# Kernel optimization log

Measured on AMD Instinct MI355X. Metric: run time of the kernel, lower is better.

The kernel has to match this reference:

```python
import jax, jax.numpy as jnp
import numpy as np


def setup_inputs() -> dict:
    key = jax.random.key(0)
    k1, k2, k3, k4 = jax.random.split(key, 4)
    B, T, C, H = 4, 4096, 1024, 64
    x = jax.random.normal(k1, (B, T, C), dtype=jnp.float32)
    Wq = jax.random.normal(k2, (C, H), dtype=jnp.float32) * (C ** -0.5)
    Wk = jax.random.normal(k3, (C, H), dtype=jnp.float32) * (C ** -0.5)
    Wv = jax.random.normal(k4, (C, H), dtype=jnp.float32) * (C ** -0.5)
    return {"x": x, "Wq": Wq, "Wk": Wk, "Wv": Wv}


def reference(x, Wq, Wk, Wv):
    B, T, C = x.shape
    q = jnp.einsum('btc,ch->bth', x, Wq)  # [B,T,H]
    k = jnp.einsum('btc,ch->bth', x, Wk)
    v = jnp.einsum('btc,ch->bth', x, Wv)
    # NOTE: original scales by C**0.5 (embed_dim), not head_size**0.5
    scale = jnp.asarray(C, x.dtype) ** 0.5
    wei = jnp.einsum('bth,bsh->bts', q, k) / scale  # [B,T,T]
    causal = jnp.tril(jnp.ones((T, T), dtype=bool))
    wei = jnp.where(causal, wei, -jnp.inf)
    wei = jax.nn.softmax(wei, axis=-1)  # dropout p=0.0 -> identity
    return jnp.einsum('bts,bsh->bth', wei, v)  # [B,T,H]
```

## Files before the change

kernel.cpp:

```cpp
#include <hip/hip_runtime.h>
#include <hip/hip_bf16.h>

typedef __bf16 bf16;
typedef __bf16 bf16x8 __attribute__((ext_vector_type(8)));
typedef __bf16 bf16x4 __attribute__((ext_vector_type(4)));
typedef float  f32x4  __attribute__((ext_vector_type(4)));

#define MFMA16(A, B, C) __builtin_amdgcn_mfma_f32_16x16x32_bf16((A), (B), (C), 0, 0, 0)

static constexpr int Bn = 4;
static constexpr int T  = 4096;
static constexpr int Cd = 1024;
static constexpr int H  = 64;
static constexpr int NG = 192;
static constexpr int CH = 8;
static constexpr int SLOTS_PER_B = 288;
static constexpr float QSCALE = 0.03125f;

__device__ inline void dma16(const void* g, void* l) {
    __builtin_amdgcn_global_load_lds(
        (const __attribute__((address_space(1))) unsigned int*)g,
        (__attribute__((address_space(3))) unsigned int*)l, 16, 0, 0);
}

__device__ inline bf16x8 cvt_bf16x8(float4 a, float4 b) {
    bf16x8 r;
    r[0] = (bf16)a.x; r[1] = (bf16)a.y; r[2] = (bf16)a.z; r[3] = (bf16)a.w;
    r[4] = (bf16)b.x; r[5] = (bf16)b.y; r[6] = (bf16)b.z; r[7] = (bf16)b.w;
    return r;
}

__global__ __launch_bounds__(256) void wt_kernel(const float* __restrict__ Wq,
                                                 const float* __restrict__ Wk,
                                                 const float* __restrict__ Wv,
                                                 bf16* __restrict__ Wt) {
    __shared__ float s[64][65];
    const int cb = blockIdx.x;
    const int m  = blockIdx.y;
    const float* W = (m == 0) ? Wq : (m == 1) ? Wk : Wv;
    for (int i = threadIdx.x; i < 64 * 64; i += 256) {
        const int c = i >> 6, h = i & 63;
        s[c][h] = W[(cb * 64 + c) * H + h];
    }
    __syncthreads();
    for (int i = threadIdx.x; i < 64 * 64; i += 256) {
        const int n = i >> 6, c = i & 63;
        Wt[(m * 64 + n) * Cd + cb * 64 + c] = (bf16)s[c][n];
    }
}

__global__ __launch_bounds__(512, 4) void proj_kernel(const float* __restrict__ x,
                                                      const bf16* __restrict__ Wt,
                                                      bf16* __restrict__ qw,
                                                      bf16* __restrict__ kw,
                                                      bf16* __restrict__ vtw) {
    const int tid  = threadIdx.x;
    const int lane = tid & 63;
    const int w    = tid >> 6;
    const int wr   = w >> 2;
    const int wc   = w & 3;
    const int ml   = lane & 15;
    const int quad = lane >> 4;

    const long r0 = (long)blockIdx.x * 32;

    __shared__ float sX[2][32][64];
    __shared__ bf16  sW[2][192][64];

    const int xrow = w * 4 + (lane >> 4);
    const float* gx = x + (r0 + xrow) * Cd + (((lane & 15) ^ (xrow & 15)) << 2);
    const int wchunk = ((lane & 7) ^ (lane >> 3)) << 3;
    const bf16* gw0 = Wt + (long)(w * 24 + 0 + (lane >> 3)) * Cd + wchunk;
    const bf16* gw1 = Wt + (long)(w * 24 + 8 + (lane >> 3)) * Cd + wchunk;
    const bf16* gw2 = Wt + (long)(w * 24 + 16 + (lane >> 3)) * Cd + wchunk;

    f32x4 acc[3];
    #pragma unroll
    for (int j = 0; j < 3; ++j) acc[j] = f32x4{0.f, 0.f, 0.f, 0.f};

    dma16(gx, &sX[0][w * 4][0]);
    dma16(gw0, &sW[0][w * 24 + 0][0]);
    dma16(gw1, &sW[0][w * 24 + 8][0]);
    dma16(gw2, &sW[0][w * 24 + 16][0]);
    __syncthreads();

    const int arow = wr * 16 + ml;
    const int brow0 = wc * 48 + ml;
    const int bsw = ml & 7;

    int buf = 0;
    for (int kb = 0; kb < Cd; kb += 64) {
        if (kb + 64 < Cd) {
            dma16(gx + kb + 64, &sX[buf ^ 1][w * 4][0]);
            dma16(gw0 + kb + 64, &sW[buf ^ 1][w * 24 + 0][0]);
            dma16(gw1 + kb + 64, &sW[buf ^ 1][w * 24 + 8][0]);
            dma16(gw2 + kb + 64, &sW[buf ^ 1][w * 24 + 16][0]);
        }

        #pragma unroll
        for (int ks = 0; ks < 2; ++ks) {
            const int ca = (ks * 8 + quad * 2) ^ ml;
            const float4 lo = *(const float4*)&sX[buf][arow][ca << 2];
            const float4 hi = *(const float4*)&sX[buf][arow][(ca ^ 1) << 2];
            const bf16x8 af = cvt_bf16x8(lo, hi);
            const int cb0 = (ks * 4 + quad) ^ bsw;
            acc[0] = MFMA16(af, *(const bf16x8*)&sW[buf][brow0 + 0][cb0 << 3], acc[0]);
            acc[1] = MFMA16(af, *(const bf16x8*)&sW[buf][brow0 + 16][cb0 << 3], acc[1]);
            acc[2] = MFMA16(af, *(const bf16x8*)&sW[buf][brow0 + 32][cb0 << 3], acc[2]);
        }

        __syncthreads();
        buf ^= 1;
    }

    const int b = (int)(r0 >> 12);
    const long rowb = r0 + wr * 16 + quad * 4;
    const int  tloc = (int)(rowb & 4095);

    #pragma unroll
    for (int f = 0; f < 3; ++f) {
        const int base = wc * 48 + f * 16;
        const int sel  = base >> 6;
        const int h    = (base & 63) + ml;
        if (sel == 0) {
            #pragma unroll
            for (int rr = 0; rr < 4; ++rr)
                qw[(rowb + rr) * H + h] = (bf16)(acc[f][rr] * QSCALE);
        } else if (sel == 1) {
            #pragma unroll
            for (int rr = 0; rr < 4; ++rr)
                kw[(rowb + rr) * H + h] = (bf16)acc[f][rr];
        } else {
            bf16x4 pv;
            #pragma unroll
            for (int rr = 0; rr < 4; ++rr) pv[rr] = (bf16)acc[f][rr];
            *(bf16x4*)(vtw + ((long)(b * H + h)) * T + tloc) = pv;
        }
    }
}

__global__ __launch_bounds__(256, 3) void attn_kernel(const bf16* __restrict__ qw,
                                                      const bf16* __restrict__ kw,
                                                      const bf16* __restrict__ vtw,
                                                      float* __restrict__ pO,
                                                      float* __restrict__ pL) {
    const int qt = blockIdx.x;
    const int c  = blockIdx.y;
    const int b  = blockIdx.z;
    const int g  = qt >> 3, r = qt & 7;
    if (c > g) return;

    const int tid  = threadIdx.x;
    const int lane = tid & 63;
    const int w    = tid >> 6;
    const int ml   = lane & 15;
    const int quad = lane >> 4;
    const int mx   = ml & 7;

    __shared__ bf16 sK[2][64][64];
    __shared__ bf16 sVt[2][64][64];
    __shared__ bf16 sP[4][16][72];

    const int t0 = qt * 64;

    const bf16* q0 = qw + ((long)b * T + t0 + w * 16 + ml) * H;
    const bf16x8 aq0 = *(const bf16x8*)(q0 + quad * 8);
    const bf16x8 aq1 = *(const bf16x8*)(q0 + 32 + quad * 8);

    f32x4 O[4];
    #pragma unroll
    for (int ht = 0; ht < 4; ++ht) O[ht] = f32x4{0.f, 0.f, 0.f, 0.f};
    float lrow[4] = {0.f, 0.f, 0.f, 0.f};

    const int trow = t0 + w * 16 + quad * 4;
    const int jt0 = c * CH;
    const int jt1 = (c == g) ? qt + 1 : (c + 1) * CH;

    const int drow = w * 8 + (lane >> 3);
    const int dsw  = ((lane & 7) ^ (drow & 7)) << 3;
    const bf16* kbase = kw + (long)b * T * H;
    const bf16* vbase = vtw + (long)b * H * T;
    const long koffA = (long)drow * H + dsw;
    const long koffB = koffA + 32 * H;
    const long voffA = (long)drow * T + dsw;
    const long voffB = voffA + (long)32 * T;

    {
        const long ks0 = (long)jt0 * 64;
        dma16(kbase + ks0 * H + koffA, &sK[0][w * 8][0]);
        dma16(kbase + ks0 * H + koffB, &sK[0][32 + w * 8][0]);
        dma16(vbase + ks0 + voffA, &sVt[0][w * 8][0]);
        dma16(vbase + ks0 + voffB, &sVt[0][32 + w * 8][0]);
    }
    __syncthreads();

    int buf = 0;
    for (int jt = jt0; jt < jt1; ++jt) {
        if (jt + 1 < jt1) {
            const long ksn = (long)(jt + 1) * 64;
            dma16(kbase + ksn * H + koffA, &sK[buf ^ 1][w * 8][0]);
            dma16(kbase + ksn * H + koffB, &sK[buf ^ 1][32 + w * 8][0]);
            dma16(vbase + ksn + voffA, &sVt[buf ^ 1][w * 8][0]);
            dma16(vbase + ksn + voffB, &sVt[buf ^ 1][32 + w * 8][0]);
        }

        const int s0 = jt * 64;
        const bool diag = (jt == qt);
        #pragma unroll
        for (int nt = 0; nt < 4; ++nt) {
            f32x4 sacc = f32x4{0.f, 0.f, 0.f, 0.f};
            sacc = MFMA16(aq0, *(const bf16x8*)&sK[buf][nt * 16 + ml][(quad ^ mx) << 3], sacc);
            sacc = MFMA16(aq1, *(const bf16x8*)&sK[buf][nt * 16 + ml][((4 + quad) ^ mx) << 3], sacc);
            const int col = s0 + nt * 16 + ml;
            #pragma unroll
            for (int rr = 0; rr < 4; ++rr) {
                const float p = (diag && col > trow + rr) ? 0.f : __expf(sacc[rr]);
                lrow[rr] += p;
                sP[w][quad * 4 + rr][nt * 16 + ml] = (bf16)p;
            }
        }
        asm volatile("s_waitcnt lgkmcnt(0)" ::: "memory");

        #pragma unroll
        for (int ks = 0; ks < 2; ++ks) {
            const bf16x8 ap = *(const bf16x8*)&sP[w][ml][ks * 32 + quad * 8];
            #pragma unroll
            for (int ht = 0; ht < 4; ++ht)
                O[ht] = MFMA16(ap,
                    *(const bf16x8*)&sVt[buf][ht * 16 + ml][(((ks << 2) + quad) ^ mx) << 3],
                    O[ht]);
        }

        __syncthreads();
        buf ^= 1;
    }

    #pragma unroll
    for (int d = 1; d < 16; d <<= 1)
        #pragma unroll
        for (int rr = 0; rr < 4; ++rr)
            lrow[rr] += __shfl_xor(lrow[rr], d, 64);

    const long slot = (long)b * SLOTS_PER_B + (long)(g + 1) * (4 * g + r) + c;
    float* po = pO + slot * 4096 + (w * 16) * 64;
    #pragma unroll
    for (int ht = 0; ht < 4; ++ht)
        #pragma unroll
        for (int rr = 0; rr < 4; ++rr)
            po[(quad * 4 + rr) * 64 + ht * 16 + ml] = O[ht][rr];
    if (ml == 0) {
        #pragma unroll
        for (int rr = 0; rr < 4; ++rr)
            pL[slot * 64 + w * 16 + quad * 4 + rr] = lrow[rr];
    }
}

__global__ __launch_bounds__(256) void combine_kernel(const float* __restrict__ pO,
                                                      const float* __restrict__ pL,
                                                      float* __restrict__ out) {
    const int qt = blockIdx.x;
    const int b  = blockIdx.y;
    const int g  = qt >> 3, r = qt & 7;
    const int nch = g + 1;
    const long slot0 = (long)b * SLOTS_PER_B + (long)(g + 1) * (4 * g + r);

    const int tid = threadIdx.x;
    const int row = tid >> 2;
    const int q4  = tid & 3;

    f32x4 o[4];
    #pragma unroll
    for (int j = 0; j < 4; ++j) o[j] = f32x4{0.f, 0.f, 0.f, 0.f};
    float l = 0.f;

    for (int cc = 0; cc < nch; ++cc) {
        const float* po = pO + (slot0 + cc) * 4096 + row * 64 + q4 * 16;
        #pragma unroll
        for (int j = 0; j < 4; ++j) o[j] += *(const f32x4*)(po + j * 4);
        l += pL[(slot0 + cc) * 64 + row];
    }
    const float inv = 1.f / l;
    float* op = out + ((long)b * T + qt * 64 + row) * H + q4 * 16;
    #pragma unroll
    for (int j = 0; j < 4; ++j) {
        f32x4 v = o[j];
        v[0] *= inv; v[1] *= inv; v[2] *= inv; v[3] *= inv;
        *(f32x4*)(op + j * 4) = v;
    }
}

extern "C" void kernel_launch(void* const* d_in, const int* in_sizes, int n_in,
                              void* d_out, int out_size, void* d_ws, size_t ws_size,
                              hipStream_t stream) {
    const float* x  = (const float*)d_in[0];
    const float* Wq = (const float*)d_in[1];
    const float* Wk = (const float*)d_in[2];
    const float* Wv = (const float*)d_in[3];
    float* out = (float*)d_out;

    char* ws = (char*)d_ws;
    const size_t WT_BYTES = (size_t)NG * Cd * sizeof(bf16);
    const size_t QK_BYTES = (size_t)Bn * T * H * sizeof(bf16);
    const size_t PO_OFF   = WT_BYTES + 3 * QK_BYTES;
    const size_t PO_BYTES = (size_t)Bn * SLOTS_PER_B * 4096 * sizeof(float);
    bf16*  Wt  = (bf16*)ws;
    bf16*  qw  = (bf16*)(ws + WT_BYTES);
    bf16*  kw  = (bf16*)(ws + WT_BYTES + QK_BYTES);
    bf16*  vtw = (bf16*)(ws + WT_BYTES + 2 * QK_BYTES);
    float* pO  = (float*)(ws + PO_OFF);
    float* pL  = (float*)(ws + PO_OFF + PO_BYTES);

    wt_kernel<<<dim3(16, 3), dim3(256), 0, stream>>>(Wq, Wk, Wv, Wt);
    proj_kernel<<<dim3((Bn * T) / 32), dim3(512), 0, stream>>>(x, Wt, qw, kw, vtw);
    attn_kernel<<<dim3(T / 64, CH, Bn), dim3(256), 0, stream>>>(qw, kw, vtw, pO, pL);
    combine_kernel<<<dim3(T / 64, Bn), dim3(256), 0, stream>>>(pO, pL, out);
}
```

Measured before the change: 153.4 us.

## Triple-buffer DMA pipelines in projection and attention, enlarge proj tile, split combine

```diff
diff --git a/kernel.cpp b/kernel.cpp
--- a/kernel.cpp
+++ b/kernel.cpp
@@ -7,6 +7,8 @@
 typedef float  f32x4  __attribute__((ext_vector_type(4)));
 
 #define MFMA16(A, B, C) __builtin_amdgcn_mfma_f32_16x16x32_bf16((A), (B), (C), 0, 0, 0)
+#define WAITV(N) asm volatile("s_waitcnt vmcnt(" #N ")" ::: "memory")
+#define BARRIER() asm volatile("s_barrier" ::: "memory")
 
 static constexpr int Bn = 4;
 static constexpr int T  = 4096;
@@ -49,7 +51,7 @@
     }
 }
 
-__global__ __launch_bounds__(512, 4) void proj_kernel(const float* __restrict__ x,
+__global__ __launch_bounds__(512, 2) void proj_kernel(const float* __restrict__ x,
                                                       const bf16* __restrict__ Wt,
                                                       bf16* __restrict__ qw,
                                                       bf16* __restrict__ kw,
@@ -62,84 +64,105 @@
     const int ml   = lane & 15;
     const int quad = lane >> 4;
 
-    const long r0 = (long)blockIdx.x * 32;
-
-    __shared__ float sX[2][32][64];
-    __shared__ bf16  sW[2][192][64];
-
-    const int xrow = w * 4 + (lane >> 4);
-    const float* gx = x + (r0 + xrow) * Cd + (((lane & 15) ^ (xrow & 15)) << 2);
-    const int wchunk = ((lane & 7) ^ (lane >> 3)) << 3;
-    const bf16* gw0 = Wt + (long)(w * 24 + 0 + (lane >> 3)) * Cd + wchunk;
-    const bf16* gw1 = Wt + (long)(w * 24 + 8 + (lane >> 3)) * Cd + wchunk;
-    const bf16* gw2 = Wt + (long)(w * 24 + 16 + (lane >> 3)) * Cd + wchunk;
-
-    f32x4 acc[3];
-    #pragma unroll
-    for (int j = 0; j < 3; ++j) acc[j] = f32x4{0.f, 0.f, 0.f, 0.f};
-
-    dma16(gx, &sX[0][w * 4][0]);
-    dma16(gw0, &sW[0][w * 24 + 0][0]);
+    const long r0 = (long)blockIdx.x * 64;
+
+    __shared__ float sX[3][64][64];
+    __shared__ bf16  sW[3][192][64];
+
+    const int xr0 = w * 8 + (lane >> 4);
+    const int xch = lane & 15;
+    const float* gx0 = x + (r0 + xr0) * Cd + ((xch ^ (xr0 & 15)) << 2);
+    const float* gx1 = x + (r0 + xr0 + 4) * Cd + ((xch ^ ((xr0 + 4) & 15)) << 2);
+    const int wr8 = lane >> 3;
+    const int wsw = ((lane & 7) ^ wr8) << 3;
+    const bf16* gw0 = Wt + (long)(w * 24 + 0  + wr8) * Cd + wsw;
+    const bf16* gw1 = Wt + (long)(w * 24 + 8  + wr8) * Cd + wsw;
+    const bf16* gw2 = Wt + (long)(w * 24 + 16 + wr8) * Cd + wsw;
+
+    f32x4 acc[2][3];
+    #pragma unroll
+    for (int g = 0; g < 2; ++g)
+        #pragma unroll
+        for (int f = 0; f < 3; ++f) acc[g][f] = f32x4{0.f, 0.f, 0.f, 0.f};
+
+    dma16(gx0, &sX[0][w * 8][0]);
+    dma16(gx1, &sX[0][w * 8 + 4][0]);
+    dma16(gw0, &sW[0][w * 24][0]);
     dma16(gw1, &sW[0][w * 24 + 8][0]);
     dma16(gw2, &sW[0][w * 24 + 16][0]);
-    __syncthreads();
-
-    const int arow = wr * 16 + ml;
-    const int brow0 = wc * 48 + ml;
-    const int bsw = ml & 7;
-
-    int buf = 0;
+    dma16(gx0 + 64, &sX[1][w * 8][0]);
+    dma16(gx1 + 64, &sX[1][w * 8 + 4][0]);
+    dma16(gw0 + 64, &sW[1][w * 24][0]);
+    dma16(gw1 + 64, &sW[1][w * 24 + 8][0]);
+    dma16(gw2 + 64, &sW[1][w * 24 + 16][0]);
+
+    int bi = 0;
     for (int kb = 0; kb < Cd; kb += 64) {
-        if (kb + 64 < Cd) {
-            dma16(gx + kb + 64, &sX[buf ^ 1][w * 4][0]);
-            dma16(gw0 + kb + 64, &sW[buf ^ 1][w * 24 + 0][0]);
-            dma16(gw1 + kb + 64, &sW[buf ^ 1][w * 24 + 8][0]);
-            dma16(gw2 + kb + 64, &sW[buf ^ 1][w * 24 + 16][0]);
+        if (kb != Cd - 64) WAITV(5);
+        else               WAITV(0);
+        BARRIER();
+        if (kb + 128 < Cd) {
+            const int bn = (bi >= 1) ? bi - 1 : 2;
+            const int kn = kb + 128;
+            dma16(gx0 + kn, &sX[bn][w * 8][0]);
+            dma16(gx1 + kn, &sX[bn][w * 8 + 4][0]);
+            dma16(gw0 + kn, &sW[bn][w * 24][0]);
+            dma16(gw1 + kn, &sW[bn][w * 24 + 8][0]);
+            dma16(gw2 + kn, &sW[bn][w * 24 + 16][0]);
         }
 
         #pragma unroll
         for (int ks = 0; ks < 2; ++ks) {
             const int ca = (ks * 8 + quad * 2) ^ ml;
-            const float4 lo = *(const float4*)&sX[buf][arow][ca << 2];
-            const float4 hi = *(const float4*)&sX[buf][arow][(ca ^ 1) << 2];
-            const bf16x8 af = cvt_bf16x8(lo, hi);
-            const int cb0 = (ks * 4 + quad) ^ bsw;
-            acc[0] = MFMA16(af, *(const bf16x8*)&sW[buf][brow0 + 0][cb0 << 3], acc[0]);
-            acc[1] = MFMA16(af, *(const bf16x8*)&sW[buf][brow0 + 16][cb0 << 3], acc[1]);
-            acc[2] = MFMA16(af, *(const bf16x8*)&sW[buf][brow0 + 32][cb0 << 3], acc[2]);
-        }
-
-        __syncthreads();
-        buf ^= 1;
+            const float4 lo0 = *(const float4*)&sX[bi][wr * 32 + ml][ca << 2];
+            const float4 hi0 = *(const float4*)&sX[bi][wr * 32 + ml][(ca ^ 1) << 2];
+            const float4 lo1 = *(const float4*)&sX[bi][wr * 32 + 16 + ml][ca << 2];
+            const float4 hi1 = *(const float4*)&sX[bi][wr * 32 + 16 + ml][(ca ^ 1) << 2];
+            const bf16x8 a0 = cvt_bf16x8(lo0, hi0);
+            const bf16x8 a1 = cvt_bf16x8(lo1, hi1);
+            const int cb0 = (ks * 4 + quad) ^ (ml & 7);
+            const bf16x8 b0 = *(const bf16x8*)&sW[bi][wc * 48 + ml][cb0 << 3];
+            const bf16x8 b1 = *(const bf16x8*)&sW[bi][wc * 48 + 16 + ml][cb0 << 3];
+            const bf16x8 b2 = *(const bf16x8*)&sW[bi][wc * 48 + 32 + ml][cb0 << 3];
+            acc[0][0] = MFMA16(a0, b0, acc[0][0]);
+            acc[0][1] = MFMA16(a0, b1, acc[0][1]);
+            acc[0][2] = MFMA16(a0, b2, acc[0][2]);
+            acc[1][0] = MFMA16(a1, b0, acc[1][0]);
+            acc[1][1] = MFMA16(a1, b1, acc[1][1]);
+            acc[1][2] = MFMA16(a1, b2, acc[1][2]);
+        }
+        bi = (bi == 2) ? 0 : bi + 1;
     }
 
     const int b = (int)(r0 >> 12);
-    const long rowb = r0 + wr * 16 + quad * 4;
-    const int  tloc = (int)(rowb & 4095);
-
-    #pragma unroll
-    for (int f = 0; f < 3; ++f) {
-        const int base = wc * 48 + f * 16;
-        const int sel  = base >> 6;
-        const int h    = (base & 63) + ml;
-        if (sel == 0) {
-            #pragma unroll
-            for (int rr = 0; rr < 4; ++rr)
-                qw[(rowb + rr) * H + h] = (bf16)(acc[f][rr] * QSCALE);
-        } else if (sel == 1) {
-            #pragma unroll
-            for (int rr = 0; rr < 4; ++rr)
-                kw[(rowb + rr) * H + h] = (bf16)acc[f][rr];
-        } else {
-            bf16x4 pv;
-            #pragma unroll
-            for (int rr = 0; rr < 4; ++rr) pv[rr] = (bf16)acc[f][rr];
-            *(bf16x4*)(vtw + ((long)(b * H + h)) * T + tloc) = pv;
-        }
-    }
-}
-
-__global__ __launch_bounds__(256, 3) void attn_kernel(const bf16* __restrict__ qw,
+    #pragma unroll
+    for (int g = 0; g < 2; ++g) {
+        const long rowb = r0 + wr * 32 + g * 16 + quad * 4;
+        const int  tloc = (int)(rowb & 4095);
+        #pragma unroll
+        for (int f = 0; f < 3; ++f) {
+            const int base = wc * 48 + f * 16;
+            const int sel  = base >> 6;
+            const int h    = (base & 63) + ml;
+            if (sel == 0) {
+                #pragma unroll
+                for (int rr = 0; rr < 4; ++rr)
+                    qw[(rowb + rr) * H + h] = (bf16)(acc[g][f][rr] * QSCALE);
+            } else if (sel == 1) {
+                #pragma unroll
+                for (int rr = 0; rr < 4; ++rr)
+                    kw[(rowb + rr) * H + h] = (bf16)acc[g][f][rr];
+            } else {
+                bf16x4 pv;
+                #pragma unroll
+                for (int rr = 0; rr < 4; ++rr) pv[rr] = (bf16)acc[g][f][rr];
+                *(bf16x4*)(vtw + ((long)(b * H + h)) * T + tloc) = pv;
+            }
+        }
+    }
+}
+
+__global__ __launch_bounds__(256, 2) void attn_kernel(const bf16* __restrict__ qw,
                                                       const bf16* __restrict__ kw,
                                                       const bf16* __restrict__ vtw,
                                                       float* __restrict__ pO,
@@ -157,8 +180,8 @@
     const int quad = lane >> 4;
     const int mx   = ml & 7;
 
-    __shared__ bf16 sK[2][64][64];
-    __shared__ bf16 sVt[2][64][64];
+    __shared__ bf16 sK[3][64][64];
+    __shared__ bf16 sVt[3][64][64];
     __shared__ bf16 sP[4][16][72];
 
     const int t0 = qt * 64;
@@ -166,6 +189,7 @@
     const bf16* q0 = qw + ((long)b * T + t0 + w * 16 + ml) * H;
     const bf16x8 aq0 = *(const bf16x8*)(q0 + quad * 8);
     const bf16x8 aq1 = *(const bf16x8*)(q0 + 32 + quad * 8);
+    WAITV(0);
 
     f32x4 O[4];
     #pragma unroll
@@ -191,17 +215,27 @@
         dma16(kbase + ks0 * H + koffB, &sK[0][32 + w * 8][0]);
         dma16(vbase + ks0 + voffA, &sVt[0][w * 8][0]);
         dma16(vbase + ks0 + voffB, &sVt[0][32 + w * 8][0]);
-    }
-    __syncthreads();
-
-    int buf = 0;
+        if (jt0 + 1 < jt1) {
+            const long ks1 = ks0 + 64;
+            dma16(kbase + ks1 * H + koffA, &sK[1][w * 8][0]);
+            dma16(kbase + ks1 * H + koffB, &sK[1][32 + w * 8][0]);
+            dma16(vbase + ks1 + voffA, &sVt[1][w * 8][0]);
+            dma16(vbase + ks1 + voffB, &sVt[1][32 + w * 8][0]);
+        }
+    }
+
+    int bi = 0;
     for (int jt = jt0; jt < jt1; ++jt) {
-        if (jt + 1 < jt1) {
-            const long ksn = (long)(jt + 1) * 64;
-            dma16(kbase + ksn * H + koffA, &sK[buf ^ 1][w * 8][0]);
-            dma16(kbase + ksn * H + koffB, &sK[buf ^ 1][32 + w * 8][0]);
-            dma16(vbase + ksn + voffA, &sVt[buf ^ 1][w * 8][0]);
-            dma16(vbase + ksn + voffB, &sVt[buf ^ 1][32 + w * 8][0]);
+        if (jt + 1 < jt1) WAITV(4);
+        else              WAITV(0);
+        BARRIER();
+        if (jt + 2 < jt1) {
+            const int bn = (bi >= 1) ? bi - 1 : 2;
+            const long ksn = (long)(jt + 2) * 64;
+            dma16(kbase + ksn * H + koffA, &sK[bn][w * 8][0]);
+            dma16(kbase + ksn * H + koffB, &sK[bn][32 + w * 8][0]);
+            dma16(vbase + ksn + voffA, &sVt[bn][w * 8][0]);
+            dma16(vbase + ksn + voffB, &sVt[bn][32 + w * 8][0]);
         }
 
         const int s0 = jt * 64;
@@ -209,8 +243,8 @@
         #pragma unroll
         for (int nt = 0; nt < 4; ++nt) {
             f32x4 sacc = f32x4{0.f, 0.f, 0.f, 0.f};
-            sacc = MFMA16(aq0, *(const bf16x8*)&sK[buf][nt * 16 + ml][(quad ^ mx) << 3], sacc);
-            sacc = MFMA16(aq1, *(const bf16x8*)&sK[buf][nt * 16 + ml][((4 + quad) ^ mx) << 3], sacc);
+            sacc = MFMA16(aq0, *(const bf16x8*)&sK[bi][nt * 16 + ml][(quad ^ mx) << 3], sacc);
+            sacc = MFMA16(aq1, *(const bf16x8*)&sK[bi][nt * 16 + ml][((4 + quad) ^ mx) << 3], sacc);
             const int col = s0 + nt * 16 + ml;
             #pragma unroll
             for (int rr = 0; rr < 4; ++rr) {
@@ -227,12 +261,10 @@
             #pragma unroll
             for (int ht = 0; ht < 4; ++ht)
                 O[ht] = MFMA16(ap,
-                    *(const bf16x8*)&sVt[buf][ht * 16 + ml][(((ks << 2) + quad) ^ mx) << 3],
+                    *(const bf16x8*)&sVt[bi][ht * 16 + ml][(((ks << 2) + quad) ^ mx) << 3],
                     O[ht]);
         }
-
-        __syncthreads();
-        buf ^= 1;
+        bi = (bi == 2) ? 0 : bi + 1;
     }
 
     #pragma unroll
@@ -260,33 +292,25 @@
                                                       float* __restrict__ out) {
     const int qt = blockIdx.x;
     const int b  = blockIdx.y;
+    const int rq = blockIdx.z;
     const int g  = qt >> 3, r = qt & 7;
     const int nch = g + 1;
     const long slot0 = (long)b * SLOTS_PER_B + (long)(g + 1) * (4 * g + r);
 
     const int tid = threadIdx.x;
-    const int row = tid >> 2;
-    const int q4  = tid & 3;
-
-    f32x4 o[4];
-    #pragma unroll
-    for (int j = 0; j < 4; ++j) o[j] = f32x4{0.f, 0.f, 0.f, 0.f};
+    const int row = rq * 16 + (tid >> 4);
+    const int c4  = (tid & 15) * 4;
+
+    f32x4 o = f32x4{0.f, 0.f, 0.f, 0.f};
     float l = 0.f;
-
     for (int cc = 0; cc < nch; ++cc) {
-        const float* po = pO + (slot0 + cc) * 4096 + row * 64 + q4 * 16;
-        #pragma unroll
-        for (int j = 0; j < 4; ++j) o[j] += *(const f32x4*)(po + j * 4);
+        o += *(const f32x4*)(pO + (slot0 + cc) * 4096 + row * 64 + c4);
         l += pL[(slot0 + cc) * 64 + row];
     }
     const float inv = 1.f / l;
-    float* op = out + ((long)b * T + qt * 64 + row) * H + q4 * 16;
-    #pragma unroll
-    for (int j = 0; j < 4; ++j) {
-        f32x4 v = o[j];
-        v[0] *= inv; v[1] *= inv; v[2] *= inv; v[3] *= inv;
-        *(f32x4*)(op + j * 4) = v;
-    }
+    f32x4 v = o;
+    v[0] *= inv; v[1] *= inv; v[2] *= inv; v[3] *= inv;
+    *(f32x4*)(out + ((long)b * T + qt * 64 + row) * H + c4) = v;
 }
 
 extern "C" void kernel_launch(void* const* d_in, const int* in_sizes, int n_in,
@@ -311,7 +335,7 @@
     float* pL  = (float*)(ws + PO_OFF + PO_BYTES);
 
     wt_kernel<<<dim3(16, 3), dim3(256), 0, stream>>>(Wq, Wk, Wv, Wt);
-    proj_kernel<<<dim3((Bn * T) / 32), dim3(512), 0, stream>>>(x, Wt, qw, kw, vtw);
+    proj_kernel<<<dim3((Bn * T) / 64), dim3(512), 0, stream>>>(x, Wt, qw, kw, vtw);
     attn_kernel<<<dim3(T / 64, CH, Bn), dim3(256), 0, stream>>>(qw, kw, vtw, pO, pL);
-    combine_kernel<<<dim3(T / 64, Bn), dim3(256), 0, stream>>>(pO, pL, out);
-}
+    combine_kernel<<<dim3(T / 64, Bn, 4), dim3(256), 0, stream>>>(pO, pL, out);
+}
```

New measurement: 159.9 us. +4.2%, slower.

## Enlarge attention query tile to 128 rows with two 16-row groups per wave

Applied to the files above, without the earlier changes.

```diff
diff --git a/kernel.cpp b/kernel.cpp
--- a/kernel.cpp
+++ b/kernel.cpp
@@ -14,7 +14,7 @@
 static constexpr int H  = 64;
 static constexpr int NG = 192;
 static constexpr int CH = 8;
-static constexpr int SLOTS_PER_B = 288;
+static constexpr int SLOTS_PER_B = 144;
 static constexpr float QSCALE = 0.03125f;
 
 __device__ inline void dma16(const void* g, void* l) {
@@ -144,11 +144,11 @@
                                                       const bf16* __restrict__ vtw,
                                                       float* __restrict__ pO,
                                                       float* __restrict__ pL) {
-    const int qt = blockIdx.x;
-    const int c  = blockIdx.y;
-    const int b  = blockIdx.z;
-    const int g  = qt >> 3, r = qt & 7;
-    if (c > g) return;
+    const int m = blockIdx.x;
+    const int c = blockIdx.y;
+    const int b = blockIdx.z;
+    const int k = (m >> 2) + 1;
+    if (c >= k) return;
 
     const int tid  = threadIdx.x;
     const int lane = tid & 63;
@@ -159,22 +159,27 @@
 
     __shared__ bf16 sK[2][64][64];
     __shared__ bf16 sVt[2][64][64];
-    __shared__ bf16 sP[4][16][72];
-
-    const int t0 = qt * 64;
-
-    const bf16* q0 = qw + ((long)b * T + t0 + w * 16 + ml) * H;
-    const bf16x8 aq0 = *(const bf16x8*)(q0 + quad * 8);
-    const bf16x8 aq1 = *(const bf16x8*)(q0 + 32 + quad * 8);
-
-    f32x4 O[4];
-    #pragma unroll
-    for (int ht = 0; ht < 4; ++ht) O[ht] = f32x4{0.f, 0.f, 0.f, 0.f};
-    float lrow[4] = {0.f, 0.f, 0.f, 0.f};
-
-    const int trow = t0 + w * 16 + quad * 4;
+    __shared__ bf16 sP[4][32][72];
+
+    const int t0  = m * 128;
+    const int wq0 = t0 + w * 32;
+
+    const bf16* qb = qw + ((long)b * T + wq0 + ml) * H;
+    const bf16x8 aq[2][2] = {
+        { *(const bf16x8*)(qb + quad * 8),          *(const bf16x8*)(qb + 32 + quad * 8) },
+        { *(const bf16x8*)(qb + 16 * H + quad * 8), *(const bf16x8*)(qb + 16 * H + 32 + quad * 8) },
+    };
+
+    f32x4 O[2][4];
+    float lrow[2][4];
+    #pragma unroll
+    for (int g = 0; g < 2; ++g)
+        #pragma unroll
+        for (int j = 0; j < 4; ++j) { O[g][j] = f32x4{0.f, 0.f, 0.f, 0.f}; lrow[g][j] = 0.f; }
+
     const int jt0 = c * CH;
-    const int jt1 = (c == g) ? qt + 1 : (c + 1) * CH;
+    const int jte = 2 * m + 2;
+    const int jt1 = ((c + 1) * CH < jte) ? (c + 1) * CH : jte;
 
     const int drow = w * 8 + (lane >> 3);
     const int dsw  = ((lane & 7) ^ (drow & 7)) << 3;
@@ -205,30 +210,38 @@
         }
 
         const int s0 = jt * 64;
-        const bool diag = (jt == qt);
-        #pragma unroll
-        for (int nt = 0; nt < 4; ++nt) {
-            f32x4 sacc = f32x4{0.f, 0.f, 0.f, 0.f};
-            sacc = MFMA16(aq0, *(const bf16x8*)&sK[buf][nt * 16 + ml][(quad ^ mx) << 3], sacc);
-            sacc = MFMA16(aq1, *(const bf16x8*)&sK[buf][nt * 16 + ml][((4 + quad) ^ mx) << 3], sacc);
-            const int col = s0 + nt * 16 + ml;
-            #pragma unroll
-            for (int rr = 0; rr < 4; ++rr) {
-                const float p = (diag && col > trow + rr) ? 0.f : __expf(sacc[rr]);
-                lrow[rr] += p;
-                sP[w][quad * 4 + rr][nt * 16 + ml] = (bf16)p;
+        if (s0 <= wq0 + 31) {
+            const bool diag = (s0 + 63 > wq0);
+            #pragma unroll
+            for (int g = 0; g < 2; ++g) {
+                const int rowb = wq0 + g * 16 + quad * 4;
+                #pragma unroll
+                for (int nt = 0; nt < 4; ++nt) {
+                    f32x4 sacc = f32x4{0.f, 0.f, 0.f, 0.f};
+                    sacc = MFMA16(aq[g][0], *(const bf16x8*)&sK[buf][nt * 16 + ml][(quad ^ mx) << 3], sacc);
+                    sacc = MFMA16(aq[g][1], *(const bf16x8*)&sK[buf][nt * 16 + ml][((4 + quad) ^ mx) << 3], sacc);
+                    const int col = s0 + nt * 16 + ml;
+                    #pragma unroll
+                    for (int rr = 0; rr < 4; ++rr) {
+                        const float p = (diag && col > rowb + rr) ? 0.f : __expf(sacc[rr]);
+                        lrow[g][rr] += p;
+                        sP[w][g * 16 + quad * 4 + rr][nt * 16 + ml] = (bf16)p;
+                    }
+                }
             }
-        }
-        asm volatile("s_waitcnt lgkmcnt(0)" ::: "memory");
-
-        #pragma unroll
-        for (int ks = 0; ks < 2; ++ks) {
-            const bf16x8 ap = *(const bf16x8*)&sP[w][ml][ks * 32 + quad * 8];
-            #pragma unroll
-            for (int ht = 0; ht < 4; ++ht)
-                O[ht] = MFMA16(ap,
-                    *(const bf16x8*)&sVt[buf][ht * 16 + ml][(((ks << 2) + quad) ^ mx) << 3],
-                    O[ht]);
+            asm volatile("s_waitcnt lgkmcnt(0)" ::: "memory");
+
+            #pragma unroll
+            for (int g = 0; g < 2; ++g)
+                #pragma unroll
+                for (int ks = 0; ks < 2; ++ks) {
+                    const bf16x8 ap = *(const bf16x8*)&sP[w][g * 16 + ml][ks * 32 + quad * 8];
+                    #pragma unroll
+                    for (int ht = 0; ht < 4; ++ht)
+                        O[g][ht] = MFMA16(ap,
+                            *(const bf16x8*)&sVt[buf][ht * 16 + ml][(((ks << 2) + quad) ^ mx) << 3],
+                            O[g][ht]);
+                }
         }
 
         __syncthreads();
@@ -238,55 +251,51 @@
     #pragma unroll
     for (int d = 1; d < 16; d <<= 1)
         #pragma unroll
-        for (int rr = 0; rr < 4; ++rr)
-            lrow[rr] += __shfl_xor(lrow[rr], d, 64);
-
-    const long slot = (long)b * SLOTS_PER_B + (long)(g + 1) * (4 * g + r) + c;
-    float* po = pO + slot * 4096 + (w * 16) * 64;
-    #pragma unroll
-    for (int ht = 0; ht < 4; ++ht)
+        for (int g = 0; g < 2; ++g)
+            #pragma unroll
+            for (int rr = 0; rr < 4; ++rr)
+                lrow[g][rr] += __shfl_xor(lrow[g][rr], d, 64);
+
+    const long slot = (long)b * SLOTS_PER_B + 2 * k * (k - 1) + (m & 3) * k + c;
+    float* po = pO + slot * 8192;
+    #pragma unroll
+    for (int g = 0; g < 2; ++g) {
         #pragma unroll
-        for (int rr = 0; rr < 4; ++rr)
-            po[(quad * 4 + rr) * 64 + ht * 16 + ml] = O[ht][rr];
-    if (ml == 0) {
-        #pragma unroll
-        for (int rr = 0; rr < 4; ++rr)
-            pL[slot * 64 + w * 16 + quad * 4 + rr] = lrow[rr];
+        for (int ht = 0; ht < 4; ++ht)
+            #pragma unroll
+            for (int rr = 0; rr < 4; ++rr)
+                po[(w * 32 + g * 16 + quad * 4 + rr) * 64 + ht * 16 + ml] = O[g][ht][rr];
+        if (ml == 0) {
+            #pragma unroll
+            for (int rr = 0; rr < 4; ++rr)
+                pL[slot * 128 + w * 32 + g * 16 + quad * 4 + rr] = lrow[g][rr];
+        }
     }
 }
 
 __global__ __launch_bounds__(256) void combine_kernel(const float* __restrict__ pO,
                                                       const float* __restrict__ pL,
                                                       float* __restrict__ out) {
-    const int qt = blockIdx.x;
+    const int m  = blockIdx.x;
     const int b  = blockIdx.y;
-    const int g  = qt >> 3, r = qt & 7;
-    const int nch = g + 1;
-    const long slot0 = (long)b * SLOTS_PER_B + (long)(g + 1) * (4 * g + r);
+    const int rq = blockIdx.z;
+    const int k  = (m >> 2) + 1;
+    const long slot0 = (long)b * SLOTS_PER_B + 2 * k * (k - 1) + (m & 3) * k;
 
     const int tid = threadIdx.x;
-    const int row = tid >> 2;
-    const int q4  = tid & 3;
-
-    f32x4 o[4];
-    #pragma unroll
-    for (int j = 0; j < 4; ++j) o[j] = f32x4{0.f, 0.f, 0.f, 0.f};
+    const int row = rq * 16 + (tid >> 4);
+    const int c4  = (tid & 15) * 4;
+
+    f32x4 o = f32x4{0.f, 0.f, 0.f, 0.f};
     float l = 0.f;
-
-    for (int cc = 0; cc < nch; ++cc) {
-        const float* po = pO + (slot0 + cc) * 4096 + row * 64 + q4 * 16;
-        #pragma unroll
-        for (int j = 0; j < 4; ++j) o[j] += *(const f32x4*)(po + j * 4);
-        l += pL[(slot0 + cc) * 64 + row];
+    for (int cc = 0; cc < k; ++cc) {
+        o += *(const f32x4*)(pO + (slot0 + cc) * 8192 + row * 64 + c4);
+        l += pL[(slot0 + cc) * 128 + row];
     }
     const float inv = 1.f / l;
-    float* op = out + ((long)b * T + qt * 64 + row) * H + q4 * 16;
-    #pragma unroll
-    for (int j = 0; j < 4; ++j) {
-        f32x4 v = o[j];
-        v[0] *= inv; v[1] *= inv; v[2] *= inv; v[3] *= inv;
-        *(f32x4*)(op + j * 4) = v;
-    }
+    f32x4 v = o;
+    v[0] *= inv; v[1] *= inv; v[2] *= inv; v[3] *= inv;
+    *(f32x4*)(out + ((long)b * T + m * 128 + row) * H + c4) = v;
 }
 
 extern "C" void kernel_launch(void* const* d_in, const int* in_sizes, int n_in,
@@ -302,7 +311,7 @@
     const size_t WT_BYTES = (size_t)NG * Cd * sizeof(bf16);
     const size_t QK_BYTES = (size_t)Bn * T * H * sizeof(bf16);
     const size_t PO_OFF   = WT_BYTES + 3 * QK_BYTES;
-    const size_t PO_BYTES = (size_t)Bn * SLOTS_PER_B * 4096 * sizeof(float);
+    const size_t PO_BYTES = (size_t)Bn * SLOTS_PER_B * 8192 * sizeof(float);
     bf16*  Wt  = (bf16*)ws;
     bf16*  qw  = (bf16*)(ws + WT_BYTES);
     bf16*  kw  = (bf16*)(ws + WT_BYTES + QK_BYTES);
@@ -312,6 +321,6 @@
 
     wt_kernel<<<dim3(16, 3), dim3(256), 0, stream>>>(Wq, Wk, Wv, Wt);
     proj_kernel<<<dim3((Bn * T) / 32), dim3(512), 0, stream>>>(x, Wt, qw, kw, vtw);
-    attn_kernel<<<dim3(T / 64, CH, Bn), dim3(256), 0, stream>>>(qw, kw, vtw, pO, pL);
-    combine_kernel<<<dim3(T / 64, Bn), dim3(256), 0, stream>>>(pO, pL, out);
-}
+    attn_kernel<<<dim3(T / 128, CH, Bn), dim3(256), 0, stream>>>(qw, kw, vtw, pO, pL);
+    combine_kernel<<<dim3(T / 128, Bn, 8), dim3(256), 0, stream>>>(pO, pL, out);
+}
```

Measured after the change: 158.2 us. 3.1% more time.

## Drop LDS K/V staging and give each wave its own 16-row causal extent

Applied to the files above, without the earlier changes.

```diff
diff --git a/kernel.cpp b/kernel.cpp
--- a/kernel.cpp
+++ b/kernel.cpp
@@ -14,7 +14,7 @@
 static constexpr int H  = 64;
 static constexpr int NG = 192;
 static constexpr int CH = 8;
-static constexpr int SLOTS_PER_B = 288;
+static constexpr int SLOTS_PER_B = 1152;
 static constexpr float QSCALE = 0.03125f;
 
 __device__ inline void dma16(const void* g, void* l) {
@@ -139,82 +139,59 @@
     }
 }
 
-__global__ __launch_bounds__(256, 3) void attn_kernel(const bf16* __restrict__ qw,
-                                                      const bf16* __restrict__ kw,
-                                                      const bf16* __restrict__ vtw,
-                                                      float* __restrict__ pO,
-                                                      float* __restrict__ pL) {
-    const int qt = blockIdx.x;
+__global__ __launch_bounds__(256) void attn_kernel(const bf16* __restrict__ qw,
+                                                   const bf16* __restrict__ kw,
+                                                   const bf16* __restrict__ vtw,
+                                                   float* __restrict__ pO,
+                                                   float* __restrict__ pL) {
+    const int bx = blockIdx.x;
     const int c  = blockIdx.y;
     const int b  = blockIdx.z;
-    const int g  = qt >> 3, r = qt & 7;
-    if (c > g) return;
+    const int kblk = (bx >> 3) + 1;
+    if (c >= kblk) return;
 
     const int tid  = threadIdx.x;
     const int lane = tid & 63;
     const int w    = tid >> 6;
     const int ml   = lane & 15;
     const int quad = lane >> 4;
-    const int mx   = ml & 7;
-
-    __shared__ bf16 sK[2][64][64];
-    __shared__ bf16 sVt[2][64][64];
+
+    const int r  = bx * 4 + w;
+    const int t0 = r * 16;
+
     __shared__ bf16 sP[4][16][72];
 
-    const int t0 = qt * 64;
-
-    const bf16* q0 = qw + ((long)b * T + t0 + w * 16 + ml) * H;
-    const bf16x8 aq0 = *(const bf16x8*)(q0 + quad * 8);
-    const bf16x8 aq1 = *(const bf16x8*)(q0 + 32 + quad * 8);
+    const bf16* qb = qw + ((long)b * T + t0 + ml) * H;
+    const bf16x8 aq0 = *(const bf16x8*)(qb + quad * 8);
+    const bf16x8 aq1 = *(const bf16x8*)(qb + 32 + quad * 8);
 
     f32x4 O[4];
     #pragma unroll
     for (int ht = 0; ht < 4; ++ht) O[ht] = f32x4{0.f, 0.f, 0.f, 0.f};
     float lrow[4] = {0.f, 0.f, 0.f, 0.f};
 
-    const int trow = t0 + w * 16 + quad * 4;
-    const int jt0 = c * CH;
-    const int jt1 = (c == g) ? qt + 1 : (c + 1) * CH;
-
-    const int drow = w * 8 + (lane >> 3);
-    const int dsw  = ((lane & 7) ^ (drow & 7)) << 3;
+    const int jdiag = r >> 2;
+    const int jt0   = c * CH;
+    const int jtmax = jdiag + 1;
+    const int jt1   = (jt0 + CH < jtmax) ? jt0 + CH : jtmax;
+
     const bf16* kbase = kw + (long)b * T * H;
     const bf16* vbase = vtw + (long)b * H * T;
-    const long koffA = (long)drow * H + dsw;
-    const long koffB = koffA + 32 * H;
-    const long voffA = (long)drow * T + dsw;
-    const long voffB = voffA + (long)32 * T;
-
-    {
-        const long ks0 = (long)jt0 * 64;
-        dma16(kbase + ks0 * H + koffA, &sK[0][w * 8][0]);
-        dma16(kbase + ks0 * H + koffB, &sK[0][32 + w * 8][0]);
-        dma16(vbase + ks0 + voffA, &sVt[0][w * 8][0]);
-        dma16(vbase + ks0 + voffB, &sVt[0][32 + w * 8][0]);
-    }
-    __syncthreads();
-
-    int buf = 0;
+
     for (int jt = jt0; jt < jt1; ++jt) {
-        if (jt + 1 < jt1) {
-            const long ksn = (long)(jt + 1) * 64;
-            dma16(kbase + ksn * H + koffA, &sK[buf ^ 1][w * 8][0]);
-            dma16(kbase + ksn * H + koffB, &sK[buf ^ 1][32 + w * 8][0]);
-            dma16(vbase + ksn + voffA, &sVt[buf ^ 1][w * 8][0]);
-            dma16(vbase + ksn + voffB, &sVt[buf ^ 1][32 + w * 8][0]);
-        }
-
         const int s0 = jt * 64;
-        const bool diag = (jt == qt);
+        const bool diag = (jt == jdiag);
+
         #pragma unroll
         for (int nt = 0; nt < 4; ++nt) {
+            const bf16* kr = kbase + (long)(s0 + nt * 16 + ml) * H + quad * 8;
             f32x4 sacc = f32x4{0.f, 0.f, 0.f, 0.f};
-            sacc = MFMA16(aq0, *(const bf16x8*)&sK[buf][nt * 16 + ml][(quad ^ mx) << 3], sacc);
-            sacc = MFMA16(aq1, *(const bf16x8*)&sK[buf][nt * 16 + ml][((4 + quad) ^ mx) << 3], sacc);
+            sacc = MFMA16(aq0, *(const bf16x8*)(kr), sacc);
+            sacc = MFMA16(aq1, *(const bf16x8*)(kr + 32), sacc);
             const int col = s0 + nt * 16 + ml;
             #pragma unroll
             for (int rr = 0; rr < 4; ++rr) {
-                const float p = (diag && col > trow + rr) ? 0.f : __expf(sacc[rr]);
+                const float p = (diag && col > t0 + quad * 4 + rr) ? 0.f : __expf(sacc[rr]);
                 lrow[rr] += p;
                 sP[w][quad * 4 + rr][nt * 16 + ml] = (bf16)p;
             }
@@ -225,14 +202,12 @@
         for (int ks = 0; ks < 2; ++ks) {
             const bf16x8 ap = *(const bf16x8*)&sP[w][ml][ks * 32 + quad * 8];
             #pragma unroll
-            for (int ht = 0; ht < 4; ++ht)
-                O[ht] = MFMA16(ap,
-                    *(const bf16x8*)&sVt[buf][ht * 16 + ml][(((ks << 2) + quad) ^ mx) << 3],
-                    O[ht]);
-        }
-
-        __syncthreads();
-        buf ^= 1;
+            for (int ht = 0; ht < 4; ++ht) {
+                const bf16x8 bv = *(const bf16x8*)(vbase + (long)(ht * 16 + ml) * T
+                                                   + s0 + ks * 32 + quad * 8);
+                O[ht] = MFMA16(ap, bv, O[ht]);
+            }
+        }
     }
 
     #pragma unroll
@@ -241,8 +216,9 @@
         for (int rr = 0; rr < 4; ++rr)
             lrow[rr] += __shfl_xor(lrow[rr], d, 64);
 
-    const long slot = (long)b * SLOTS_PER_B + (long)(g + 1) * (4 * g + r) + c;
-    float* po = pO + slot * 4096 + (w * 16) * 64;
+    const int G = r >> 5;
+    const long slot = (long)b * SLOTS_PER_B + 16 * G * (G + 1) + (long)(r & 31) * (G + 1) + c;
+    float* po = pO + slot * 1024;
     #pragma unroll
     for (int ht = 0; ht < 4; ++ht)
         #pragma unroll
@@ -251,42 +227,33 @@
     if (ml == 0) {
         #pragma unroll
         for (int rr = 0; rr < 4; ++rr)
-            pL[slot * 64 + w * 16 + quad * 4 + rr] = lrow[rr];
+            pL[slot * 16 + quad * 4 + rr] = lrow[rr];
     }
 }
 
 __global__ __launch_bounds__(256) void combine_kernel(const float* __restrict__ pO,
                                                       const float* __restrict__ pL,
                                                       float* __restrict__ out) {
-    const int qt = blockIdx.x;
-    const int b  = blockIdx.y;
-    const int g  = qt >> 3, r = qt & 7;
-    const int nch = g + 1;
-    const long slot0 = (long)b * SLOTS_PER_B + (long)(g + 1) * (4 * g + r);
+    const int r = blockIdx.x;
+    const int b = blockIdx.y;
+    const int G = r >> 5;
+    const int k = G + 1;
+    const long slot0 = (long)b * SLOTS_PER_B + 16 * G * (G + 1) + (long)(r & 31) * k;
 
     const int tid = threadIdx.x;
-    const int row = tid >> 2;
-    const int q4  = tid & 3;
-
-    f32x4 o[4];
-    #pragma unroll
-    for (int j = 0; j < 4; ++j) o[j] = f32x4{0.f, 0.f, 0.f, 0.f};
+    const int row = tid >> 4;
+    const int c4  = (tid & 15) * 4;
+
+    f32x4 o = f32x4{0.f, 0.f, 0.f, 0.f};
     float l = 0.f;
-
-    for (int cc = 0; cc < nch; ++cc) {
-        const float* po = pO + (slot0 + cc) * 4096 + row * 64 + q4 * 16;
-        #pragma unroll
-        for (int j = 0; j < 4; ++j) o[j] += *(const f32x4*)(po + j * 4);
-        l += pL[(slot0 + cc) * 64 + row];
+    for (int cc = 0; cc < k; ++cc) {
+        o += *(const f32x4*)(pO + (slot0 + cc) * 1024 + row * 64 + c4);
+        l += pL[(slot0 + cc) * 16 + row];
     }
     const float inv = 1.f / l;
-    float* op = out + ((long)b * T + qt * 64 + row) * H + q4 * 16;
-    #pragma unroll
-    for (int j = 0; j < 4; ++j) {
-        f32x4 v = o[j];
-        v[0] *= inv; v[1] *= inv; v[2] *= inv; v[3] *= inv;
-        *(f32x4*)(op + j * 4) = v;
-    }
+    f32x4 v = o;
+    v[0] *= inv; v[1] *= inv; v[2] *= inv; v[3] *= inv;
+    *(f32x4*)(out + ((long)b * T + r * 16 + row) * H + c4) = v;
 }
 
 extern "C" void kernel_launch(void* const* d_in, const int* in_sizes, int n_in,
@@ -302,7 +269,7 @@
     const size_t WT_BYTES = (size_t)NG * Cd * sizeof(bf16);
     const size_t QK_BYTES = (size_t)Bn * T * H * sizeof(bf16);
     const size_t PO_OFF   = WT_BYTES + 3 * QK_BYTES;
-    const size_t PO_BYTES = (size_t)Bn * SLOTS_PER_B * 4096 * sizeof(float);
+    const size_t PO_BYTES = (size_t)Bn * SLOTS_PER_B * 1024 * sizeof(float);
     bf16*  Wt  = (bf16*)ws;
     bf16*  qw  = (bf16*)(ws + WT_BYTES);
     bf16*  kw  = (bf16*)(ws + WT_BYTES + QK_BYTES);
@@ -312,6 +279,6 @@
 
     wt_kernel<<<dim3(16, 3), dim3(256), 0, stream>>>(Wq, Wk, Wv, Wt);
     proj_kernel<<<dim3((Bn * T) / 32), dim3(512), 0, stream>>>(x, Wt, qw, kw, vtw);
-    attn_kernel<<<dim3(T / 64, CH, Bn), dim3(256), 0, stream>>>(qw, kw, vtw, pO, pL);
-    combine_kernel<<<dim3(T / 64, Bn), dim3(256), 0, stream>>>(pO, pL, out);
-}
+    attn_kernel<<<dim3(64, CH, Bn), dim3(256), 0, stream>>>(qw, kw, vtw, pO, pL);
+    combine_kernel<<<dim3(256, Bn), dim3(256), 0, stream>>>(pO, pL, out);
+}
```

After: 231.2 us. 1.51x slower.
